# Kernel tuning notes

Hardware: AMD Instinct MI355X
Metric: run time of the kernel (lower is better)

## Reference

```python
import jax, jax.numpy as jnp
import numpy as np

KSIZE, STRIDE, SCALE = 7, 4, 10.0


def _same_pad_amounts(n, k, s):
    out = -(-n // s)
    pad = max(0, (out - 1) * s + k - n)
    return pad // 2, pad - pad // 2, out


def _conv(x, w, b, stride=1, pad=0):
    y = jax.lax.conv_general_dilated(
        x, w, (stride, stride), [(pad, pad), (pad, pad)],
        dimension_numbers=("NCHW", "OIHW", "NCHW"))
    return y + b[None, :, None, None]


def setup_inputs() -> dict:
    key = jax.random.key(0)
    ks = jax.random.split(key, 10)
    B, Cin, H, W = 2, 64, 256, 256
    Ci = 16                       # inter_channels
    d_in = KSIZE * KSIZE * Ci     # 784 = ksize^2 * inter_channels
    d_out = d_in // 4             # 196
    s = 0.02
    return {
        "b": jax.random.normal(ks[0], (B, Cin, H, W), jnp.float32),
        "g_w": jax.random.normal(ks[1], (Ci, Cin, 3, 3), jnp.float32) * s,
        "g_b": jnp.zeros((Ci,), jnp.float32),
        "theta_w": jax.random.normal(ks[2], (Ci, Cin, 1, 1), jnp.float32) * s,
        "theta_b": jnp.zeros((Ci,), jnp.float32),
        "W_w": jax.random.normal(ks[3], (Cin, Ci, 1, 1), jnp.float32) * s,
        "W_b": jnp.zeros((Cin,), jnp.float32),
        "fc1_w": jax.random.normal(ks[4], (d_out, d_in), jnp.float32) * s,
        "fc1_b": jnp.zeros((d_out,), jnp.float32),
        "fc2_w": jax.random.normal(ks[5], (d_out, d_in), jnp.float32) * s,
        "fc2_b": jnp.zeros((d_out,), jnp.float32),
        "thr_w": jax.random.normal(ks[6], (1, Cin, KSIZE, KSIZE), jnp.float32) * s,
        "thr_b": jnp.zeros((1,), jnp.float32),
        "bias_w": jax.random.normal(ks[7], (1, Cin, KSIZE, KSIZE), jnp.float32) * s,
        "bias_b": jnp.zeros((1,), jnp.float32),
    }


def _forward(b, g_w, g_b, theta_w, theta_b, W_w, W_b, fc1_w, fc1_b,
             fc2_w, fc2_b, thr_w, thr_b, bias_w, bias_b):
    B, Cin, H, W = b.shape
    k, s = KSIZE, STRIDE
    pt, pb, Lh = _same_pad_amounts(H, k, s)
    pl, pr, Lw = _same_pad_amounts(W, k, s)
    L = Lh * Lw
    Ci = g_w.shape[0]

    b1 = _conv(b, g_w, g_b, 1, 1)            # [B,Ci,H,W]
    b2 = _conv(b, theta_w, theta_b, 1, 0)    # [B,Ci,H,W]
    b4 = jnp.pad(b, ((0, 0), (0, 0), (pt, pb), (pl, pr)))
    thr = _conv(b4, thr_w, thr_b, s, 0).reshape(B, L)   # per-patch threshold
    bias = _conv(b4, bias_w, bias_b, s, 0).reshape(B, L)  # per-patch bias

    # patch gather indices on the 'same'-padded grid (torch.Unfold order)
    R = (jnp.arange(Lh) * s)[:, None] + jnp.arange(k)[None, :]   # [Lh,k]
    Cc = (jnp.arange(Lw) * s)[:, None] + jnp.arange(k)[None, :]  # [Lw,k]
    Ri = R[:, None, :, None]                                     # -> [Lh,Lw,k,k]
    Cj = Cc[None, :, None, :]

    def patches(x):  # [B,Ci,H,W] -> [B,L,Ci*k*k], flatten order (C,kh,kw)
        xp = jnp.pad(x, ((0, 0), (0, 0), (pt, pb), (pl, pr)))
        p = xp[:, :, Ri, Cj]                       # [B,Ci,Lh,Lw,k,k]
        return p.transpose(0, 2, 3, 1, 4, 5).reshape(B, L, -1)

    wi = patches(b1)     # stride_1 patches of b1
    xi = wi              # b3 = b1 and stride_1 == stride_2 -> identical patches
    pi = patches(b2)     # stride_2 patches of b2, values to aggregate

    wi_f = jax.nn.relu(jnp.einsum("bld,od->blo", wi, fc1_w) + fc1_b)
    xi_f = jax.nn.relu(jnp.einsum("bld,od->blo", xi, fc2_w) + fc2_b)
    score = jnp.einsum("blo,bmo->blm", wi_f, xi_f)   # [B,L,L] patch similarity

    # threshold-gated sparse attention with learned per-patch thr/bias
    mask = (score >= thr[:, :, None]).astype(score.dtype)
    gated = score * mask + bias[:, :, None]
    attn = jax.nn.softmax(gated * SCALE, axis=-1) * mask
    attn = attn / (attn.sum(-1, keepdims=True) + 1e-8)

    agg = jnp.einsum("blm,bmd->bld", attn, pi)       # [B,L,Ci*k*k]
    p6 = agg.reshape(B, Lh, Lw, Ci, k, k).transpose(0, 3, 1, 2, 4, 5)

    # fold back (sum overlaps), normalize by overlap count, crop padding
    Hp, Wp = H + pt + pb, W + pl + pr
    folded = jnp.zeros((B, Ci, Hp, Wp), score.dtype).at[:, :, Ri, Cj].add(p6)
    cnt = jnp.zeros((Hp, Wp), score.dtype).at[Ri, Cj].add(1.0)
    zi = (folded / cnt)[:, :, pl:pl + H, pt:pt + W]

    return b + _conv(zi, W_w, W_b, 1, 0)


def reference(b, g_w, g_b, theta_w, theta_b, W_w, W_b, fc1_w, fc1_b,
              fc2_w, fc2_b, thr_w, thr_b, bias_w, bias_b):
    return _forward(b, g_w, g_b, theta_w, theta_b, W_w, W_b, fc1_w, fc1_b,
                    fc2_w, fc2_b, thr_w, thr_b, bias_w, bias_b)
```

## Files before the change

### kernel.cpp

```cpp
#include <hip/hip_runtime.h>
#include <math.h>

#define CIN  64
#define CI   16
#define HH   256
#define WWD  256
#define KS   7
#define STR  4
#define LH   64
#define LWD  64
#define LL   4096
#define DIN  784
#define DINP 896
#define DKP  832
#define DOUT 196
#define DOUTP 256
#define NB   2
#define YP   258
#define XP   264

typedef __attribute__((ext_vector_type(8))) short bf16x8;
typedef __attribute__((ext_vector_type(4))) float f32x4;
typedef __attribute__((ext_vector_type(16))) float f32x16;
typedef __attribute__((ext_vector_type(8))) int i32x8;
typedef __attribute__((ext_vector_type(4))) int i32x4;

__device__ __forceinline__ unsigned short f2bf(float x) {
    unsigned int u = __float_as_uint(x);
    unsigned int r = (u + 0x7FFFu + ((u >> 16) & 1u)) >> 16;
    return (unsigned short)r;
}
__device__ __forceinline__ float bf2f(unsigned short h) {
    return __uint_as_float(((unsigned int)h) << 16);
}

__device__ __forceinline__ void stage16(const void* g, void* l) {
#if defined(__has_builtin)
#if __has_builtin(__builtin_amdgcn_global_load_lds)
    __builtin_amdgcn_global_load_lds(
        (const __attribute__((address_space(1))) unsigned int*)g,
        (__attribute__((address_space(3))) unsigned int*)l, 16, 0, 0);
    return;
#endif
#endif
    *(float4*)l = *(const float4*)g;
}

__global__ __launch_bounds__(256) void k_prep_b(const float* __restrict__ b,
                                                unsigned short* __restrict__ bTp) {
    int blk = blockIdx.x;
    int s = blk & 7; int yy = (blk >> 3) % YP; int n = blk / (8 * YP);
    int y = yy - 1;
    for (int xx = threadIdx.x; xx < XP; xx += 256) {
        int x = xx - 4;
        bool v = (y >= 0 && y < 256 && x >= 0 && x < 256);
        unsigned short h[8];
#pragma unroll
        for (int j = 0; j < 8; j++)
            h[j] = v ? f2bf(b[((size_t)(n * 64 + s * 8 + j) * 256 + y) * 256 + x]) : (unsigned short)0;
        *(uint4*)&bTp[((((size_t)n * YP + yy) * 8 + s) * XP + xx) * 8] = *(uint4*)h;
    }
}

__global__ void k_prep_wb(const float* __restrict__ g_w, const float* __restrict__ th_w,
                          unsigned short* __restrict__ wbt) {
    int i = blockIdx.x * 256 + threadIdx.x;
    if (i >= 18432) return;
    int j = i & 7, co = (i >> 3) & 31, q = (i >> 8) & 3, h = (i >> 10) & 1, t = i >> 11;
    int ci = h * 32 + q * 8 + j;
    float v;
    if (co < 16) v = g_w[((size_t)co * 64 + ci) * 9 + t];
    else         v = (t == 4) ? th_w[(size_t)(co - 16) * 64 + ci] : 0.f;
    wbt[i] = f2bf(v);
}

__global__ void k_prep_fc(const float* __restrict__ fc1_w, const float* __restrict__ fc2_w,
                          unsigned short* __restrict__ fcwb) {
    int i = blockIdx.x * 256 + threadIdx.x;
    if (i >= 2 * DOUTP * DKP) return;
    int col = i % DKP; int row = (i / DKP) % DOUTP; int f = i / (DKP * DOUTP);
    float v = 0.f;
    if (row < DOUT && col < DIN) v = (f ? fc2_w : fc1_w)[row * DIN + col];
    fcwb[i] = f2bf(v);
}

__global__ __launch_bounds__(256) void k_convm(
        const unsigned short* __restrict__ bTp, const unsigned short* __restrict__ wbt,
        const float* __restrict__ g_b, const float* __restrict__ th_b,
        unsigned short* __restrict__ bx) {
    __shared__ unsigned short wb[18432];
    __shared__ unsigned short ti[8 * 3 * 68 * 8];
    int tid = threadIdx.x;
#pragma unroll
    for (int i = 0; i < 9; i++) {
        int c = i * 256 + tid;
        stage16(wbt + (size_t)c * 8, &wb[c * 8]);
    }
    int n = blockIdx.x >> 8, y = blockIdx.x & 255;
    int wave = tid >> 6, lane = tid & 63, lr = lane & 15, q = lane >> 4;
    int m0 = wave * 16;
    float bg = g_b[lr], bt = th_b[lr];
    for (int xs = 0; xs < 4; xs++) {
        __syncthreads();
        int x0 = xs * 64;
#pragma unroll
        for (int i = 0; i < 7; i++) {
            int c = i * 256 + tid;
            if (c < 1632) {
                int s = c / 204; int rem = c % 204; int r = rem / 68; int cc = rem % 68;
                const unsigned short* src =
                    bTp + ((((size_t)n * YP + y + r) * 8 + s) * XP + (x0 + 3 + cc)) * 8;
                stage16(src, &ti[c * 8]);
            }
        }
        __syncthreads();
        f32x4 a0 = {bg, bg, bg, bg}, a1 = {bt, bt, bt, bt};
#pragma unroll
        for (int t = 0; t < 9; t++) {
            int dy = t / 3, dx = t % 3;
#pragma unroll
            for (int h = 0; h < 2; h++) {
                int s = h * 4 + q;
                bf16x8 av = *(const bf16x8*)&ti[(((s * 3 + dy) * 68) + m0 + lr + dx) * 8];
                bf16x8 b0 = *(const bf16x8*)&wb[((((t * 2 + h) * 4 + q) * 32) + lr) * 8];
                bf16x8 b1 = *(const bf16x8*)&wb[((((t * 2 + h) * 4 + q) * 32) + 16 + lr) * 8];
                a0 = __builtin_amdgcn_mfma_f32_16x16x32_bf16(av, b0, a0, 0, 0, 0);
                a1 = __builtin_amdgcn_mfma_f32_16x16x32_bf16(av, b1, a1, 0, 0, 0);
            }
        }
        size_t pb = (((size_t)n * 256 + y) * 256 + x0 + m0 + q * 4);
#pragma unroll
        for (int r = 0; r < 4; r++) {
            bx[(pb + r) * 32 + lr]      = f2bf(a0[r]);
            bx[(pb + r) * 32 + 16 + lr] = f2bf(a1[r]);
        }
    }
}

__global__ __launch_bounds__(256) void k_thr(
        const unsigned short* __restrict__ bTp, const float* __restrict__ thr_w,
        const float* __restrict__ thr_b, float* __restrict__ thr) {
    __shared__ float w[64 * 49];
    int tid = threadIdx.x;
    for (int i = tid; i < 64 * 49; i += 256) w[i] = thr_w[i];
    __syncthreads();
    int wid = (blockIdx.x << 2) + (tid >> 6);
    int lane = tid & 63;
    int s = lane >> 3, j = lane & 7;
    int n = wid >> 12, l = wid & 4095;
    int lh = (l >> 6), lw = l & 63;
    const float* wl = w + (s * 8 + j) * 49;
    float acc = 0.f;
#pragma unroll
    for (int dy = 0; dy < 7; dy++) {
        int yy = lh * 4 + dy;
        if (yy >= YP) continue;
        const unsigned short* row = bTp + (((size_t)(n * YP + yy) * 8 + s) * XP) * 8;
#pragma unroll
        for (int dx = 0; dx < 7; dx++) {
            int xx = lw * 4 + dx + 3;
            acc = fmaf(bf2f(row[xx * 8 + j]), wl[dy * 7 + dx], acc);
        }
    }
#pragma unroll
    for (int off = 32; off > 0; off >>= 1) acc += __shfl_down(acc, off, 64);
    if (lane == 0) thr[wid] = acc + thr_b[0];
}

__global__ void k_patchesA(const unsigned short* __restrict__ bx, unsigned short* __restrict__ Pb) {
    size_t e = (size_t)blockIdx.x * 256 + threadIdx.x;
    if (e >= (size_t)NB * LL * DKP) return;
    int d = (int)(e % DKP); size_t r = e / DKP;
    int l = (int)(r & 4095); int n = (int)(r >> 12);
    unsigned short v = 0;
    if (d < DIN) {
        int ci = d / 49; int t = d % 49; int dy = t / 7; int dx = t % 7;
        int y = (l >> 6) * 4 + dy - 1, x = (l & 63) * 4 + dx - 1;
        if (y >= 0 && y < 256 && x >= 0 && x < 256)
            v = bx[(((size_t)n * 256 + y) * 256 + x) * 32 + ci];
    }
    Pb[e] = v;
}

__global__ void k_patchesT(const unsigned short* __restrict__ bx, unsigned char* __restrict__ piT8) {
    size_t e = (size_t)blockIdx.x * 256 + threadIdx.x;
    int l = (int)(e & 4095);
    int d = (int)((e >> 12) % DINP);
    int n = (int)(e / ((size_t)DINP * LL));
    float v = 0.f;
    if (d < DIN) {
        int ci = d / 49; int t = d % 49; int dy = t / 7; int dx = t % 7;
        int y = (l >> 6) * 4 + dy - 1, x = (l & 63) * 4 + dx - 1;
        if (y >= 0 && y < 256 && x >= 0 && x < 256)
            v = bf2f(bx[(((size_t)n * 256 + y) * 256 + x) * 32 + 16 + ci]);
    }
    int p = __builtin_amdgcn_cvt_pk_fp8_f32(v, 0.f, 0, false);
    piT8[e] = (unsigned char)(p & 0xFF);
}

template<int MODE>
__global__ __launch_bounds__(256) void k_gemm_nt(
        const unsigned short* __restrict__ A, const unsigned short* __restrict__ Bt,
        void* __restrict__ C, int lda, int ldb, int ldc, int K,
        size_t sA, size_t sB, size_t sC,
        const float* __restrict__ bias1, const float* __restrict__ bias2) {
    __shared__ unsigned short lA[128 * 64];
    __shared__ unsigned short lB[128 * 64];
    int tid = threadIdx.x;
    int wave = tid >> 6, lane = tid & 63;
    int lr = lane & 15, lq = lane >> 4;
    int wm = (wave >> 1) * 64, wn = (wave & 1) * 64;
    int i0 = blockIdx.x * 128, j0 = blockIdx.y * 128;
    int z = blockIdx.z;
    int az = (MODE == 2) ? (z >> 1) : z;
    int bz = (MODE == 2) ? (z & 1) : z;
    const unsigned short* Ab = A + (size_t)az * sA + (size_t)i0 * lda;
    const unsigned short* Bb = Bt + (size_t)bz * sB + (size_t)j0 * ldb;
    f32x4 acc[4][4] = {};
    for (int k0 = 0; k0 < K; k0 += 64) {
        __syncthreads();
#pragma unroll
        for (int it = 0; it < 4; it++) {
            int c = it * 256 + tid;
            int row = c >> 3, slot = c & 7;
            int col8 = slot ^ (row & 7);
            stage16(Ab + (size_t)row * lda + k0 + col8 * 8, &lA[c * 8]);
        }
#pragma unroll
        for (int it = 0; it < 4; it++) {
            int c = it * 256 + tid;
            int row = c >> 3, slot = c & 7;
            int col8 = slot ^ (row & 7);
            stage16(Bb + (size_t)row * ldb + k0 + col8 * 8, &lB[c * 8]);
        }
        __syncthreads();
#pragma unroll
        for (int ks = 0; ks < 2; ks++) {
            bf16x8 af[4], bfr[4];
#pragma unroll
            for (int t = 0; t < 4; t++) {
                int row = wm + t * 16 + lr;
                int slot = ks * 4 + lq;
                af[t] = *(const bf16x8*)&lA[row * 64 + (slot ^ (row & 7)) * 8];
            }
#pragma unroll
            for (int t = 0; t < 4; t++) {
                int row = wn + t * 16 + lr;
                int slot = ks * 4 + lq;
                bfr[t] = *(const bf16x8*)&lB[row * 64 + (slot ^ (row & 7)) * 8];
            }
#pragma unroll
            for (int mi = 0; mi < 4; mi++)
#pragma unroll
                for (int nj = 0; nj < 4; nj++)
                    acc[mi][nj] = __builtin_amdgcn_mfma_f32_16x16x32_bf16(
                        af[mi], bfr[nj], acc[mi][nj], 0, 0, 0);
        }
    }
    if (MODE == 1) {
        unsigned short* Cb = (unsigned short*)C + (size_t)z * sC;
#pragma unroll
        for (int mi = 0; mi < 4; mi++)
#pragma unroll
            for (int r = 0; r < 4; r++) {
                int row = i0 + wm + mi * 16 + lq * 4 + r;
#pragma unroll
                for (int nj = 0; nj < 4; nj++)
                    Cb[(size_t)row * ldc + j0 + wn + nj * 16 + lr] = f2bf(acc[mi][nj][r]);
            }
    } else {
        const float* biasp = bz ? bias2 : bias1;
        unsigned short* Cb = (unsigned short*)C + (size_t)z * sC;
#pragma unroll
        for (int mi = 0; mi < 4; mi++)
#pragma unroll
            for (int r = 0; r < 4; r++) {
                int row = i0 + wm + mi * 16 + lq * 4 + r;
#pragma unroll
                for (int nj = 0; nj < 4; nj++) {
                    int col = j0 + wn + nj * 16 + lr;
                    float bv = (col < DOUT) ? biasp[col] : 0.f;
                    float v = fmaxf(acc[mi][nj][r] + bv, 0.f);
                    Cb[(size_t)row * ldc + col] = f2bf(v);
                }
            }
    }
}

__global__ __launch_bounds__(256) void k_gemm_mx(
        const unsigned char* __restrict__ A, const unsigned char* __restrict__ Bt,
        unsigned short* __restrict__ C, int lda, int ldb, int ldc, int K,
        size_t sA, size_t sB, size_t sC) {
    __shared__ unsigned char lA[2][128 * 128];
    __shared__ unsigned char lB[2][128 * 128];
    int tid = threadIdx.x;
    int wave = tid >> 6, lane = tid & 63;
    int lr = lane & 31, hf = lane >> 5;
    int wm = (wave >> 1) * 64, wn = (wave & 1) * 64;
    int i0 = blockIdx.x * 128, j0 = blockIdx.y * 128;
    int z = blockIdx.z;
    const unsigned char* Ab = A + (size_t)z * sA + (size_t)i0 * lda;
    const unsigned char* Bb = Bt + (size_t)z * sB + (size_t)j0 * ldb;

    auto stageAB = [&](int buf, int k0) {
#pragma unroll
        for (int it = 0; it < 4; it++) {
            int c = it * 256 + tid;
            int row = c >> 3, slot = c & 7;
            int col16 = slot ^ ((row ^ (row >> 3)) & 7);
            stage16(Ab + (size_t)row * lda + k0 + col16 * 16, &lA[buf][c * 16]);
        }
#pragma unroll
        for (int it = 0; it < 4; it++) {
            int c = it * 256 + tid;
            int row = c >> 3, slot = c & 7;
            int col16 = slot ^ ((row ^ (row >> 3)) & 7);
            stage16(Bb + (size_t)row * ldb + k0 + col16 * 16, &lB[buf][c * 16]);
        }
    };

    f32x16 acc[2][2] = {};
    int NT = K >> 7;
    stageAB(0, 0);
    stageAB(1, 128);
    for (int t = 0; t < NT; ++t) {
        int cur = t & 1;
        if (t + 1 < NT) { asm volatile("s_waitcnt vmcnt(8)" ::: "memory"); }
        else           { asm volatile("s_waitcnt vmcnt(0)" ::: "memory"); }
        __builtin_amdgcn_s_barrier();
        asm volatile("" ::: "memory");
#pragma unroll
        for (int kk = 0; kk < 2; kk++) {
            i32x8 af[2], bfv[2];
            int c0 = kk * 4 + hf * 2;
#pragma unroll
            for (int t2 = 0; t2 < 2; t2++) {
                int row = wm + t2 * 32 + lr;
                int sw = (row ^ (row >> 3)) & 7;
                i32x4 lo = *(const i32x4*)&lA[cur][row * 128 + ((c0    ) ^ sw) * 16];
                i32x4 hi = *(const i32x4*)&lA[cur][row * 128 + ((c0 + 1) ^ sw) * 16];
                af[t2][0] = lo[0]; af[t2][1] = lo[1]; af[t2][2] = lo[2]; af[t2][3] = lo[3];
                af[t2][4] = hi[0]; af[t2][5] = hi[1]; af[t2][6] = hi[2]; af[t2][7] = hi[3];
            }
#pragma unroll
            for (int t2 = 0; t2 < 2; t2++) {
                int row = wn + t2 * 32 + lr;
                int sw = (row ^ (row >> 3)) & 7;
                i32x4 lo = *(const i32x4*)&lB[cur][row * 128 + ((c0    ) ^ sw) * 16];
                i32x4 hi = *(const i32x4*)&lB[cur][row * 128 + ((c0 + 1) ^ sw) * 16];
                bfv[t2][0] = lo[0]; bfv[t2][1] = lo[1]; bfv[t2][2] = lo[2]; bfv[t2][3] = lo[3];
                bfv[t2][4] = hi[0]; bfv[t2][5] = hi[1]; bfv[t2][6] = hi[2]; bfv[t2][7] = hi[3];
            }
#pragma unroll
            for (int mi = 0; mi < 2; mi++)
#pragma unroll
                for (int nj = 0; nj < 2; nj++)
                    acc[mi][nj] = __builtin_amdgcn_mfma_scale_f32_32x32x64_f8f6f4(
                        af[mi], bfv[nj], acc[mi][nj],
                        0, 0,
                        0, 0x7F7F7F7F,
                        0, 0x7F7F7F7F);
        }
        asm volatile("s_waitcnt lgkmcnt(0)" ::: "memory");
        __builtin_amdgcn_s_barrier();
        if (t + 2 < NT) stageAB(cur, (t + 2) << 7);
    }
    unsigned short* Cb = C + (size_t)z * sC;
#pragma unroll
    for (int mi = 0; mi < 2; mi++)
#pragma unroll
        for (int nj = 0; nj < 2; nj++)
#pragma unroll
            for (int reg = 0; reg < 16; reg++) {
                int row = i0 + wm + mi * 32 + (reg & 3) + 8 * (reg >> 2) + 4 * hf;
                int col = j0 + wn + nj * 32 + lr;
                Cb[(size_t)row * ldc + col] = f2bf(acc[mi][nj][reg]);
            }
}

__global__ __launch_bounds__(256) void k_softmax(
        const unsigned short* __restrict__ score, const float* __restrict__ thr,
        unsigned char* __restrict__ attn8) {
    __shared__ uint4 srow[512];
    __shared__ float red[256], red2[256];
    int row = blockIdx.x, tid = threadIdx.x;
    const uint4* g4 = (const uint4*)(score + (size_t)row * LL);
    float t = thr[row];
    float mx = 0.f;
#pragma unroll
    for (int c = tid; c < 512; c += 256) {
        uint4 u = g4[c];
        srow[c] = u;
        unsigned int w[4] = {u.x, u.y, u.z, u.w};
#pragma unroll
        for (int qq = 0; qq < 4; qq++) {
            float v0 = __uint_as_float(w[qq] << 16);
            float v1 = __uint_as_float(w[qq] & 0xFFFF0000u);
            if (v0 >= t) mx = fmaxf(mx, v0);
            if (v1 >= t) mx = fmaxf(mx, v1);
        }
    }
    red[tid] = mx; __syncthreads();
    for (int st = 128; st > 0; st >>= 1) {
        if (tid < st) red[tid] = fmaxf(red[tid], red[tid + st]);
        __syncthreads();
    }
    float M = 10.f * fmaxf(red[0], 0.f);
    __syncthreads();
    float s2 = 0.f, n0 = 0.f;
#pragma unroll
    for (int c = tid; c < 512; c += 256) {
        uint4 u = srow[c];
        unsigned int w[4] = {u.x, u.y, u.z, u.w};
#pragma unroll
        for (int qq = 0; qq < 4; qq++) {
            float v0 = __uint_as_float(w[qq] << 16);
            float v1 = __uint_as_float(w[qq] & 0xFFFF0000u);
            if (v0 >= t) s2 += __expf(10.f * v0 - M); else n0 += 1.f;
            if (v1 >= t) s2 += __expf(10.f * v1 - M); else n0 += 1.f;
        }
    }
    red[tid] = s2; red2[tid] = n0; __syncthreads();
    for (int st = 128; st > 0; st >>= 1) {
        if (tid < st) { red[tid] += red[tid + st]; red2[tid] += red2[tid + st]; }
        __syncthreads();
    }
    float S2 = red[0], N0 = red2[0];
    float iD = 1.f / (S2 + 1e-8f * (S2 + N0 * __expf(-M)));
#pragma unroll
    for (int c = tid; c < 512; c += 256) {
        uint4 u = srow[c];
        unsigned int w[4] = {u.x, u.y, u.z, u.w};
        float a[8];
#pragma unroll
        for (int qq = 0; qq < 4; qq++) {
            float v0 = __uint_as_float(w[qq] << 16);
            float v1 = __uint_as_float(w[qq] & 0xFFFF0000u);
            a[2 * qq]     = (v0 >= t) ? __expf(10.f * v0 - M) * iD : 0.f;
            a[2 * qq + 1] = (v1 >= t) ? __expf(10.f * v1 - M) * iD : 0.f;
        }
        int d0 = __builtin_amdgcn_cvt_pk_fp8_f32(a[0], a[1], 0, false);
        d0     = __builtin_amdgcn_cvt_pk_fp8_f32(a[2], a[3], d0, true);
        int d1 = __builtin_amdgcn_cvt_pk_fp8_f32(a[4], a[5], 0, false);
        d1     = __builtin_amdgcn_cvt_pk_fp8_f32(a[6], a[7], d1, true);
        *(uint2*)&attn8[(size_t)row * LL + c * 8] = make_uint2((unsigned)d0, (unsigned)d1);
    }
}

__global__ void k_fold(const unsigned short* __restrict__ aggb, float* __restrict__ zi) {
    int p = blockIdx.x * 256 + threadIdx.x;
    int x = p & 255, y = (p >> 8) & 255, ci = (p >> 16) & 15, n = p >> 20;
    int yp = y + 1, xp = x + 1;
    int lh1 = yp >> 2; if (lh1 > 63) lh1 = 63;
    int lh0 = (yp >= 3) ? ((yp - 3) >> 2) : 0;
    int lw1 = xp >> 2; if (lw1 > 63) lw1 = 63;
    int lw0 = (xp >= 3) ? ((xp - 3) >> 2) : 0;
    const unsigned short* a0 = aggb + (size_t)n * LL * DINP;
    float sum = 0.f;
    for (int lh = lh0; lh <= lh1; lh++) {
        int dy = yp - 4 * lh;
        for (int lw = lw0; lw <= lw1; lw++) {
            int dx = xp - 4 * lw;
            sum += bf2f(a0[(size_t)(lh * 64 + lw) * DINP + ci * 49 + dy * 7 + dx]);
        }
    }
    float cnt = (float)((lh1 - lh0 + 1) * (lw1 - lw0 + 1));
    zi[p] = sum / cnt;
}

__global__ void k_final(const float* __restrict__ zi, const float* __restrict__ b,
                        const float* __restrict__ W_w, const float* __restrict__ W_b,
                        float* __restrict__ out) {
    __shared__ float w[16 * 64];
    int tid = threadIdx.x;
    for (int i = tid; i < 16 * 64; i += 256) {
        int ci = i >> 6; int co = i & 63;
        w[i] = W_w[co * 16 + ci];
    }
    __syncthreads();
    int p = blockIdx.x * 256 + tid;
    int n = p >> 16, yx = p & 65535;
    float acc[64];
#pragma unroll
    for (int co = 0; co < 64; co++) acc[co] = 0.f;
    const float* zn = zi + (size_t)n * 16 * 65536;
#pragma unroll
    for (int ci = 0; ci < 16; ci++) {
        float v = zn[ci * 65536 + yx];
#pragma unroll
        for (int co = 0; co < 64; co++) acc[co] += v * w[ci * 64 + co];
    }
    const float* bn = b + (size_t)n * 64 * 65536;
    float* on = out + (size_t)n * 64 * 65536;
#pragma unroll
    for (int co = 0; co < 64; co++) on[co * 65536 + yx] = bn[co * 65536 + yx] + acc[co] + W_b[co];
}

extern "C" void kernel_launch(void* const* d_in, const int* in_sizes, int n_in,
                              void* d_out, int out_size, void* d_ws, size_t ws_size,
                              hipStream_t stream) {
    const float* b     = (const float*)d_in[0];
    const float* g_w   = (const float*)d_in[1];
    const float* g_b   = (const float*)d_in[2];
    const float* th_w  = (const float*)d_in[3];
    const float* th_b  = (const float*)d_in[4];
    const float* W_w   = (const float*)d_in[5];
    const float* W_b   = (const float*)d_in[6];
    const float* fc1_w = (const float*)d_in[7];
    const float* fc1_b = (const float*)d_in[8];
    const float* fc2_w = (const float*)d_in[9];
    const float* fc2_b = (const float*)d_in[10];
    const float* thr_w = (const float*)d_in[11];
    const float* thr_b = (const float*)d_in[12];
    float* out = (float*)d_out;

    float* ws = (float*)d_ws;
    size_t off = 0;
    auto alloc = [&](size_t nf) { float* p = ws + off; off += (nf + 63) & ~(size_t)63; return p; };
    unsigned short* aggb = (unsigned short*)alloc((size_t)NB * LL * DINP / 2);
    float* zi   = alloc((size_t)NB * CI * HH * WWD);
    unsigned short* bTp  = (unsigned short*)alloc((size_t)NB * YP * 8 * XP * 8 / 2);
    unsigned short* bx   = (unsigned short*)alloc((size_t)NB * HH * WWD * 32 / 2);
    unsigned short* Pb   = (unsigned short*)alloc((size_t)NB * LL * DKP / 2);
    unsigned char*  piT8 = (unsigned char*)alloc((size_t)NB * DINP * LL / 4);
    unsigned short* fcout = (unsigned short*)alloc((size_t)NB * 2 * LL * DOUTP / 2);
    unsigned short* wbt  = (unsigned short*)alloc(18432 / 2);
    unsigned short* fcwb = (unsigned short*)alloc((size_t)2 * DOUTP * DKP / 2);
    float* thr  = alloc((size_t)NB * LL);
    unsigned short* score = (unsigned short*)alloc((size_t)NB * LL * LL / 2);
    unsigned char*  attn8 = (unsigned char*)alloc((size_t)NB * LL * LL / 4);

    k_prep_b<<<dim3(NB * YP * 8), 256, 0, stream>>>(b, bTp);
    k_prep_wb<<<dim3(72), 256, 0, stream>>>(g_w, th_w, wbt);
    k_prep_fc<<<dim3((2 * DOUTP * DKP + 255) / 256), 256, 0, stream>>>(fc1_w, fc2_w, fcwb);
    k_convm<<<dim3(NB * 256), 256, 0, stream>>>(bTp, wbt, g_b, th_b, bx);
    k_thr<<<dim3(2048), 256, 0, stream>>>(bTp, thr_w, thr_b, thr);
    k_patchesA<<<dim3((int)((size_t)NB * LL * DKP / 256)), 256, 0, stream>>>(bx, Pb);
    k_patchesT<<<dim3((int)((size_t)NB * DINP * LL / 256)), 256, 0, stream>>>(bx, piT8);
    k_gemm_nt<2><<<dim3(32, 2, 4), 256, 0, stream>>>(
        Pb, fcwb, (void*)fcout, DKP, DKP, DOUTP, DKP,
        (size_t)LL * DKP, (size_t)DOUTP * DKP, (size_t)LL * DOUTP, fc1_b, fc2_b);
    k_gemm_nt<1><<<dim3(32, 32, NB), 256, 0, stream>>>(
        fcout, fcout + (size_t)LL * DOUTP, (void*)score, DOUTP, DOUTP, LL, DOUTP,
        (size_t)2 * LL * DOUTP, (size_t)2 * LL * DOUTP, (size_t)LL * LL, nullptr, nullptr);
    k_softmax<<<dim3(NB * LL), 256, 0, stream>>>(score, thr, attn8);
    k_gemm_mx<<<dim3(32, DINP / 128, NB), 256, 0, stream>>>(
        attn8, piT8, aggb, LL, LL, DINP, LL,
        (size_t)LL * LL, (size_t)DINP * LL, (size_t)LL * DINP);
    k_fold<<<dim3(8192), 256, 0, stream>>>(aggb, zi);
    k_final<<<dim3(512), 256, 0, stream>>>(zi, b, W_w, W_b, out);
}
```

Measured before the change: 328.4 us.

## Double-buffer LDS in bf16 GEMM and keep softmax row in registers

The generic NT GEMM now uses two LDS buffers per operand and prefetches tile t+2 while computing tile t. Partial vmcnt waits and raw barriers replace the full __syncthreads pairs, so global loads overlap with MFMA work. Separately, the softmax kernel holds its 16 values per thread in registers, computing each exp once and reusing it instead of rereading shared memory and recomputing exponentials. The cost is double the LDS footprint in the GEMM, which can lower occupancy, and a correctness risk from the hand-counted vmcnt(8) matching exactly 8 outstanding loads per stage.

```diff
diff --git a/kernel.cpp b/kernel.cpp
--- a/kernel.cpp
+++ b/kernel.cpp
@@ -204,8 +204,8 @@
         void* __restrict__ C, int lda, int ldb, int ldc, int K,
         size_t sA, size_t sB, size_t sC,
         const float* __restrict__ bias1, const float* __restrict__ bias2) {
-    __shared__ unsigned short lA[128 * 64];
-    __shared__ unsigned short lB[128 * 64];
+    __shared__ unsigned short lA[2][128 * 64];
+    __shared__ unsigned short lB[2][128 * 64];
     int tid = threadIdx.x;
     int wave = tid >> 6, lane = tid & 63;
     int lr = lane & 15, lq = lane >> 4;
@@ -216,38 +216,47 @@
     int bz = (MODE == 2) ? (z & 1) : z;
     const unsigned short* Ab = A + (size_t)az * sA + (size_t)i0 * lda;
     const unsigned short* Bb = Bt + (size_t)bz * sB + (size_t)j0 * ldb;
-    f32x4 acc[4][4] = {};
-    for (int k0 = 0; k0 < K; k0 += 64) {
-        __syncthreads();
+
+    auto stageAB = [&](int buf, int k0) {
 #pragma unroll
         for (int it = 0; it < 4; it++) {
             int c = it * 256 + tid;
             int row = c >> 3, slot = c & 7;
             int col8 = slot ^ (row & 7);
-            stage16(Ab + (size_t)row * lda + k0 + col8 * 8, &lA[c * 8]);
+            stage16(Ab + (size_t)row * lda + k0 + col8 * 8, &lA[buf][c * 8]);
         }
 #pragma unroll
         for (int it = 0; it < 4; it++) {
             int c = it * 256 + tid;
             int row = c >> 3, slot = c & 7;
             int col8 = slot ^ (row & 7);
-            stage16(Bb + (size_t)row * ldb + k0 + col8 * 8, &lB[c * 8]);
-        }
-        __syncthreads();
+            stage16(Bb + (size_t)row * ldb + k0 + col8 * 8, &lB[buf][c * 8]);
+        }
+    };
+
+    f32x4 acc[4][4] = {};
+    int NT = K >> 6;
+    stageAB(0, 0);
+    stageAB(1, 64);
+    for (int t = 0; t < NT; ++t) {
+        int cur = t & 1;
+        if (t + 1 < NT) { asm volatile("s_waitcnt vmcnt(8)" ::: "memory"); }
+        else            { asm volatile("s_waitcnt vmcnt(0)" ::: "memory"); }
+        __builtin_amdgcn_s_barrier();
 #pragma unroll
         for (int ks = 0; ks < 2; ks++) {
             bf16x8 af[4], bfr[4];
 #pragma unroll
-            for (int t = 0; t < 4; t++) {
-                int row = wm + t * 16 + lr;
+            for (int t2 = 0; t2 < 4; t2++) {
+                int row = wm + t2 * 16 + lr;
                 int slot = ks * 4 + lq;
-                af[t] = *(const bf16x8*)&lA[row * 64 + (slot ^ (row & 7)) * 8];
-            }
-#pragma unroll
-            for (int t = 0; t < 4; t++) {
-                int row = wn + t * 16 + lr;
+                af[t2] = *(const bf16x8*)&lA[cur][row * 64 + (slot ^ (row & 7)) * 8];
+            }
+#pragma unroll
+            for (int t2 = 0; t2 < 4; t2++) {
+                int row = wn + t2 * 16 + lr;
                 int slot = ks * 4 + lq;
-                bfr[t] = *(const bf16x8*)&lB[row * 64 + (slot ^ (row & 7)) * 8];
+                bfr[t2] = *(const bf16x8*)&lB[cur][row * 64 + (slot ^ (row & 7)) * 8];
             }
 #pragma unroll
             for (int mi = 0; mi < 4; mi++)
@@ -256,6 +265,9 @@
                     acc[mi][nj] = __builtin_amdgcn_mfma_f32_16x16x32_bf16(
                         af[mi], bfr[nj], acc[mi][nj], 0, 0, 0);
         }
+        asm volatile("s_waitcnt lgkmcnt(0)" ::: "memory");
+        __builtin_amdgcn_s_barrier();
+        if (t + 2 < NT) stageAB(cur, (t + 2) << 6);
     }
     if (MODE == 1) {
         unsigned short* Cb = (unsigned short*)C + (size_t)z * sC;
@@ -381,25 +393,23 @@
 __global__ __launch_bounds__(256) void k_softmax(
         const unsigned short* __restrict__ score, const float* __restrict__ thr,
         unsigned char* __restrict__ attn8) {
-    __shared__ uint4 srow[512];
     __shared__ float red[256], red2[256];
     int row = blockIdx.x, tid = threadIdx.x;
     const uint4* g4 = (const uint4*)(score + (size_t)row * LL);
     float t = thr[row];
+    uint4 u0 = g4[tid], u1 = g4[tid + 256];
+    float v[16];
+    {
+        unsigned int w[8] = {u0.x, u0.y, u0.z, u0.w, u1.x, u1.y, u1.z, u1.w};
+#pragma unroll
+        for (int q = 0; q < 8; q++) {
+            v[2 * q]     = __uint_as_float(w[q] << 16);
+            v[2 * q + 1] = __uint_as_float(w[q] & 0xFFFF0000u);
+        }
+    }
     float mx = 0.f;
 #pragma unroll
-    for (int c = tid; c < 512; c += 256) {
-        uint4 u = g4[c];
-        srow[c] = u;
-        unsigned int w[4] = {u.x, u.y, u.z, u.w};
-#pragma unroll
-        for (int qq = 0; qq < 4; qq++) {
-            float v0 = __uint_as_float(w[qq] << 16);
-            float v1 = __uint_as_float(w[qq] & 0xFFFF0000u);
-            if (v0 >= t) mx = fmaxf(mx, v0);
-            if (v1 >= t) mx = fmaxf(mx, v1);
-        }
-    }
+    for (int k = 0; k < 16; k++) if (v[k] >= t) mx = fmaxf(mx, v[k]);
     red[tid] = mx; __syncthreads();
     for (int st = 128; st > 0; st >>= 1) {
         if (tid < st) red[tid] = fmaxf(red[tid], red[tid + st]);
@@ -407,18 +417,12 @@
     }
     float M = 10.f * fmaxf(red[0], 0.f);
     __syncthreads();
+    float e[16];
     float s2 = 0.f, n0 = 0.f;
 #pragma unroll
-    for (int c = tid; c < 512; c += 256) {
-        uint4 u = srow[c];
-        unsigned int w[4] = {u.x, u.y, u.z, u.w};
-#pragma unroll
-        for (int qq = 0; qq < 4; qq++) {
-            float v0 = __uint_as_float(w[qq] << 16);
-            float v1 = __uint_as_float(w[qq] & 0xFFFF0000u);
-            if (v0 >= t) s2 += __expf(10.f * v0 - M); else n0 += 1.f;
-            if (v1 >= t) s2 += __expf(10.f * v1 - M); else n0 += 1.f;
-        }
+    for (int k = 0; k < 16; k++) {
+        if (v[k] >= t) { e[k] = __expf(10.f * v[k] - M); s2 += e[k]; }
+        else           { e[k] = 0.f; n0 += 1.f; }
     }
     red[tid] = s2; red2[tid] = n0; __syncthreads();
     for (int st = 128; st > 0; st >>= 1) {
@@ -428,22 +432,13 @@
     float S2 = red[0], N0 = red2[0];
     float iD = 1.f / (S2 + 1e-8f * (S2 + N0 * __expf(-M)));
 #pragma unroll
-    for (int c = tid; c < 512; c += 256) {
-        uint4 u = srow[c];
-        unsigned int w[4] = {u.x, u.y, u.z, u.w};
-        float a[8];
-#pragma unroll
-        for (int qq = 0; qq < 4; qq++) {
-            float v0 = __uint_as_float(w[qq] << 16);
-            float v1 = __uint_as_float(w[qq] & 0xFFFF0000u);
-            a[2 * qq]     = (v0 >= t) ? __expf(10.f * v0 - M) * iD : 0.f;
-            a[2 * qq + 1] = (v1 >= t) ? __expf(10.f * v1 - M) * iD : 0.f;
-        }
-        int d0 = __builtin_amdgcn_cvt_pk_fp8_f32(a[0], a[1], 0, false);
-        d0     = __builtin_amdgcn_cvt_pk_fp8_f32(a[2], a[3], d0, true);
-        int d1 = __builtin_amdgcn_cvt_pk_fp8_f32(a[4], a[5], 0, false);
-        d1     = __builtin_amdgcn_cvt_pk_fp8_f32(a[6], a[7], d1, true);
-        *(uint2*)&attn8[(size_t)row * LL + c * 8] = make_uint2((unsigned)d0, (unsigned)d1);
+    for (int i = 0; i < 2; i++) {
+        int c = tid + i * 256;
+        int d0 = __builtin_amdgcn_cvt_pk_fp8_f32(e[i * 8 + 0] * iD, e[i * 8 + 1] * iD, 0, false);
+        d0     = __builtin_amdgcn_cvt_pk_fp8_f32(e[i * 8 + 2] * iD, e[i * 8 + 3] * iD, d0, true);
+        int d1 = __builtin_amdgcn_cvt_pk_fp8_f32(e[i * 8 + 4] * iD, e[i * 8 + 5] * iD, 0, false);
+        d1     = __builtin_amdgcn_cvt_pk_fp8_f32(e[i * 8 + 6] * iD, e[i * 8 + 7] * iD, d1, true);
+        *(uint2*)&attn8[(size_t)row * LL + (size_t)c * 8] = make_uint2((unsigned)d0, (unsigned)d1);
     }
 }
 
```

Result: no change. 323.0 us (-1.6%).
